# Kernel optimization log

Hardware: AMD Instinct MI355X
Metric: run time of the kernel (lower is better)

The kernel has to match this reference:

```python
import jax, jax.numpy as jnp
import numpy as np

N_K = 20000; N_E = 50000; N_U = 100000; EMB = 128
E_UND = 200000; E_EK = 400000; E_EU = 600000


def _gat(h, W, a, src, dst, n):
    """RCD GraphLayer: single-head GAT with edge softmax over incoming edges."""
    z = h @ W                                  # [N, d]
    d = z.shape[1]
    el = z @ a[:d]                             # src contribution to attn logit
    er = z @ a[d:]                             # dst contribution
    e = jax.nn.leaky_relu(el[src] + er[dst], 0.01)   # [E]
    m = jax.ops.segment_max(e, dst, num_segments=n)
    m = jnp.where(jnp.isfinite(m), m, 0.0)     # guard zero-degree nodes
    ex = jnp.exp(e - m[dst])
    s = jax.ops.segment_sum(ex, dst, num_segments=n)
    alpha = ex / s[dst]                        # per-dst softmax weights [E]
    return jax.ops.segment_sum(alpha[:, None] * z[src], dst, num_segments=n)


def setup_inputs() -> dict:
    key = jax.random.key(0)
    ks = jax.random.split(key, 32)
    sc = 1.0 / np.sqrt(EMB)
    inp = {
        'kn_emb': jax.random.normal(ks[0], (N_K, EMB), jnp.float32),
        'exer_emb': jax.random.normal(ks[1], (N_E, EMB), jnp.float32),
        'all_stu_emb': jax.random.normal(ks[2], (N_U, EMB), jnp.float32),
        'und_src': jax.random.randint(ks[3], (E_UND,), 0, N_K),
        'und_dst': jax.random.randint(ks[4], (E_UND,), 0, N_K),
        'ek_src': jax.random.randint(ks[5], (E_EK,), 0, N_E),
        'ek_dst': jax.random.randint(ks[6], (E_EK,), 0, N_K),
        'eu_src': jax.random.randint(ks[7], (E_EU,), 0, N_E),
        'eu_dst': jax.random.randint(ks[8], (E_EU,), 0, N_U),
        'W_und': jax.random.normal(ks[9], (EMB, EMB), jnp.float32) * sc,
        'a_und': jax.random.normal(ks[10], (2 * EMB,), jnp.float32) * sc,
        'W_ek': jax.random.normal(ks[11], (EMB, EMB), jnp.float32) * sc,
        'a_ek': jax.random.normal(ks[12], (2 * EMB,), jnp.float32) * sc,
        'W_ke': jax.random.normal(ks[13], (EMB, EMB), jnp.float32) * sc,
        'a_ke': jax.random.normal(ks[14], (2 * EMB,), jnp.float32) * sc,
        'W_eu': jax.random.normal(ks[15], (EMB, EMB), jnp.float32) * sc,
        'a_eu': jax.random.normal(ks[16], (2 * EMB,), jnp.float32) * sc,
        'W_ue': jax.random.normal(ks[17], (EMB, EMB), jnp.float32) * sc,
        'a_ue': jax.random.normal(ks[18], (2 * EMB,), jnp.float32) * sc,
        'k_fc2_w': jax.random.normal(ks[19], (2 * EMB,), jnp.float32) * sc,
        'k_fc2_b': jnp.zeros((1,), jnp.float32),
        'k_fc3_w': jax.random.normal(ks[20], (2 * EMB,), jnp.float32) * sc,
        'k_fc3_b': jnp.zeros((1,), jnp.float32),
        'e_fc1_w': jax.random.normal(ks[21], (2 * EMB,), jnp.float32) * sc,
        'e_fc1_b': jnp.zeros((1,), jnp.float32),
        'e_fc2_w': jax.random.normal(ks[22], (2 * EMB,), jnp.float32) * sc,
        'e_fc2_b': jnp.zeros((1,), jnp.float32),
    }
    return inp


def reference(kn_emb, exer_emb, all_stu_emb, und_src, und_dst, ek_src, ek_dst,
              eu_src, eu_dst, W_und, a_und, W_ek, a_ek, W_ke, a_ke, W_eu, a_eu,
              W_ue, a_ue, k_fc2_w, k_fc2_b, k_fc3_w, k_fc3_b, e_fc1_w, e_fc1_b,
              e_fc2_w, e_fc2_b):
    d = EMB
    # 1) undirected GAT on knowledge graph
    k_und = _gat(kn_emb, W_und, a_und, und_src, und_dst, N_K)
    # 2) exercise<->knowledge graphs on concatenated [exer; kn] nodes
    ek_nodes = jnp.concatenate([exer_emb, kn_emb], axis=0)
    e2k = _gat(ek_nodes, W_ek, a_ek, ek_src, ek_dst + N_E, N_E + N_K)
    k2e = _gat(ek_nodes, W_ke, a_ke, ek_dst + N_E, ek_src, N_E + N_K)
    # 3) exercise<->student graphs on concatenated [exer; stu] nodes
    eu_nodes = jnp.concatenate([exer_emb, all_stu_emb], axis=0)
    e2u = _gat(eu_nodes, W_eu, a_eu, eu_src, eu_dst + N_E, N_E + N_U)
    u2e = _gat(eu_nodes, W_ue, a_ue, eu_dst + N_E, eu_src, N_E + N_U)
    # knowledge fusion: attention-weighted residual combination
    A = kn_emb; C = k_und; D = e2k[N_E:]
    s2 = A @ k_fc2_w[:d] + C @ k_fc2_w[d:] + k_fc2_b[0]
    s3 = A @ k_fc3_w[:d] + D @ k_fc3_w[d:] + k_fc3_b[0]
    sk = jax.nn.softmax(jnp.stack([s2, s3], axis=1), axis=1)
    kn_out = A + sk[:, 0:1] * C + sk[:, 1:2] * D
    # exercise fusion
    Ae = exer_emb; B = k2e[:N_E]; Ce = u2e[:N_E]
    s1 = Ae @ e_fc1_w[:d] + B @ e_fc1_w[d:] + e_fc1_b[0]
    s2e = Ae @ e_fc2_w[:d] + Ce @ e_fc2_w[d:] + e_fc2_b[0]
    se = jax.nn.softmax(jnp.stack([s1, s2e], axis=1), axis=1)
    exer_out = Ae + se[:, 0:1] * B + se[:, 1:2] * Ce
    # student residual
    stu_out = all_stu_emb + e2u[N_E:]
    return (kn_out, exer_out, stu_out)
```

## Files before the change

kernel.cpp:

```cpp
#include <hip/hip_runtime.h>

#define N_K 20000
#define N_E 50000
#define N_U 100000
#define E_TOT 2200000
#define N_TOT 240000
#define KB1 0
#define KB2 20000
#define KB3 40000
#define KB4 90000
#define KB5 190000
#define NBKT 726
#define EPB 8192
#define NBLKA 269
#define APAD 272
#define KN_B 1250
#define EX_B 3125
#define ST_B 6250

typedef unsigned short u16;
typedef unsigned int u32;
typedef __bf16 bf16x8 __attribute__((ext_vector_type(8)));
typedef float f32x4 __attribute__((ext_vector_type(4)));

__device__ __forceinline__ float bf2f(u16 v){
    union { u32 u; float f; } x; x.u = ((u32)v) << 16; return x.f;
}
__device__ __forceinline__ u16 f2bf(float f){
    union { float f; u32 u; } x; x.f = f;
    u32 r = x.u + 0x7FFFu + ((x.u >> 16) & 1u);
    return (u16)(r >> 16);
}
__device__ __forceinline__ float leaky_exp(float x){
    x = x >= 0.f ? x : 0.01f*x;
    return __expf(x);
}

__device__ __forceinline__ int bucket_of(int key){
    if (key < 20000)  return key >> 8;
    if (key < 40000)  return 79  + ((key - 20000) >> 7);
    if (key < 90000)  return 236 + ((key - 40000) >> 9);
    if (key < 190000) return 334 + ((key - 90000) >> 9);
    return 530 + ((key - 190000) >> 8);
}
__device__ __forceinline__ void bucket_info(int b, int& kb, int& w, int& r){
    if (b < 79){       r=0; kb = b << 8;                 w = min(256, 20000  - kb); }
    else if (b < 236){ r=1; kb = 20000 + ((b-79)  << 7); w = min(128, 40000  - kb); }
    else if (b < 334){ r=2; kb = 40000 + ((b-236) << 9); w = min(512, 90000  - kb); }
    else if (b < 530){ r=3; kb = 90000 + ((b-334) << 9); w = min(512, 190000 - kb); }
    else {             r=4; kb = 190000 + ((b-530) << 8); w = min(256, 240000 - kb); }
}
__device__ __forceinline__ int edge_key(int e,
    const int* ud, const int* es, const int* ed, const int* vs, const int* vd){
    if (e < 200000)  return ud[e];
    if (e < 600000)  return 20000  + ed[e-200000];
    if (e < 1000000) return 40000  + es[e-600000];
    if (e < 1600000) return 90000  + vd[e-1000000];
    return 190000 + vs[e-1600000];
}
__device__ __forceinline__ int edge_src(int e,
    const int* us, const int* es, const int* ed, const int* vs, const int* vd){
    if (e < 200000)  return us[e];
    if (e < 600000)  return es[e-200000];
    if (e < 1000000) return ed[e-600000];
    if (e < 1600000) return vs[e-1000000];
    return vd[e-1600000];
}

__global__ __launch_bounds__(256) void prep_w(
    const float* W0, const float* W1, const float* W2, const float* W3, const float* W4,
    const float* a0, const float* a1, const float* a2, const float* a3, const float* a4,
    float* __restrict__ vecs, u16* __restrict__ Wf)
{
    int bid = blockIdx.x;
    if (bid < 320){
        int o = bid*4 + (threadIdx.x >> 6);
        int lane = threadIdx.x & 63;
        int which = o / 640, rem = o - which*640, g = rem >> 7, k = rem & 127;
        const float* W = g==0?W0:g==1?W1:g==2?W2:g==3?W3:W4;
        const float* a = g==0?a0:g==1?a1:g==2?a2:g==3?a3:a4;
        const float* av = a + which*128;
        int c = lane*2;
        float s = W[k*128 + c]*av[c] + W[k*128 + c + 1]*av[c+1];
        #pragma unroll
        for (int m = 32; m; m >>= 1) s += __shfl_xor(s, m);
        if (lane == 0) vecs[(which*5 + g)*128 + k] = s;
    } else {
        int t = (bid - 320)*256 + threadIdx.x;
        int g = t / 2048, i = t - g*2048;
        const float* W = g==0?W0:g==1?W1:g==2?W2:g==3?W3:W4;
        int lane = i & 63, tt = i >> 6, ks = tt & 3, ct = tt >> 2;
        int kbase = ks*32 + (lane>>4)*8;
        int c = ct*16 + (lane&15);
        #pragma unroll
        for (int j = 0; j < 8; ++j)
            Wf[g*16384 + i*8 + j] = f2bf(W[(kbase+j)*128 + c]);
    }
}

template<int WBF>
__global__ __launch_bounds__(256) void conv_all(
    const float* __restrict__ kn, const float* __restrict__ exer, const float* __restrict__ stu,
    u16* __restrict__ knb, u16* __restrict__ exerb, u16* __restrict__ stub,
    const float* __restrict__ vecs,
    float* __restrict__ el1, float* __restrict__ el2, float* __restrict__ el3,
    float* __restrict__ el4, float* __restrict__ el5, float* __restrict__ erc)
{
    int w = (int)((blockIdx.x*(u32)blockDim.x + threadIdx.x) >> 6);
    int lane = threadIdx.x & 63;
    if (w >= 170000) return;
    const float* h; u16* hb; int local, nd;
    const float *v0,*v1,*v2,*v3;
    float *o0,*o1,*o2,*o3;
    if (w < 20000){
        local = w; h = kn; hb = knb; nd = 4;
        v0=vecs+0;    v1=vecs+640;  v2=vecs+768;  v3=vecs+256;
        o0=el1; o1=erc+KB1; o2=erc+KB2; o3=el3;
    } else if (w < 70000){
        local = w - 20000; h = exer; hb = exerb; nd = 4;
        v0=vecs+128;  v1=vecs+896;  v2=vecs+384;  v3=vecs+1152;
        o0=el2; o1=erc+KB3; o2=el4; o3=erc+KB5;
    } else {
        local = w - 70000; h = stu; hb = stub; nd = 2;
        v0=vecs+1024; v1=vecs+512;  v2=vecs;      v3=vecs;
        o0=erc+KB4; o1=el5; o2=nullptr; o3=nullptr;
    }
    float2 hv = *(const float2*)(h + (size_t)local*128 + lane*2);
    if (WBF)
        *(u32*)(hb + (size_t)local*128 + lane*2) = (u32)f2bf(hv.x) | ((u32)f2bf(hv.y) << 16);
    int c = lane*2;
    float d0 = hv.x*v0[c] + hv.y*v0[c+1];
    float d1 = hv.x*v1[c] + hv.y*v1[c+1];
    float d2 = hv.x*v2[c] + hv.y*v2[c+1];
    float d3 = hv.x*v3[c] + hv.y*v3[c+1];
    #pragma unroll
    for (int o = 32; o; o >>= 1){
        d0 += __shfl_xor(d0, o); d1 += __shfl_xor(d1, o);
        d2 += __shfl_xor(d2, o); d3 += __shfl_xor(d3, o);
    }
    if (lane == 0){
        o0[local] = d0; o1[local] = d1;
        if (nd == 4){ o2[local] = d2; o3[local] = d3; }
    }
}

__global__ __launch_bounds__(256) void bkt_hist(
    const int* __restrict__ ud, const int* __restrict__ es, const int* __restrict__ ed,
    const int* __restrict__ vs, const int* __restrict__ vd, int* __restrict__ hist)
{
    __shared__ int h[NBKT];
    for (int i = threadIdx.x; i < NBKT; i += 256) h[i] = 0;
    __syncthreads();
    int base = blockIdx.x * EPB;
    #pragma unroll 4
    for (int it = 0; it < EPB/256; ++it){
        int e = base + it*256 + threadIdx.x;
        if (e < E_TOT){
            int key = edge_key(e, ud, es, ed, vs, vd);
            atomicAdd(&h[bucket_of(key)], 1);
        }
    }
    __syncthreads();
    for (int i = threadIdx.x; i < NBKT; i += 256)
        hist[i*APAD + blockIdx.x] = h[i];
}

__global__ __launch_bounds__(512) void bkt_scan1(int* __restrict__ hist, int* __restrict__ btot)
{
    __shared__ int sm[512];
    int t = threadIdx.x;
    int v = (t < NBLKA) ? hist[blockIdx.x*APAD + t] : 0;
    sm[t] = v; __syncthreads();
    #pragma unroll
    for (int d = 1; d < 512; d <<= 1){
        int x = (t >= d) ? sm[t-d] : 0;
        __syncthreads();
        sm[t] += x;
        __syncthreads();
    }
    if (t < NBLKA) hist[blockIdx.x*APAD + t] = sm[t] - v;
    if (t == 511) btot[blockIdx.x] = sm[511];
}

__global__ __launch_bounds__(1024) void bkt_scan2(const int* __restrict__ btot, int* __restrict__ bbase)
{
    __shared__ int sm[1024];
    int t = threadIdx.x;
    int v = (t < NBKT) ? btot[t] : 0;
    sm[t] = v; __syncthreads();
    #pragma unroll
    for (int d = 1; d < 1024; d <<= 1){
        int x = (t >= d) ? sm[t-d] : 0;
        __syncthreads();
        sm[t] += x;
        __syncthreads();
    }
    if (t < NBKT) bbase[t] = sm[t] - v;
}

__global__ __launch_bounds__(256) void bkt_scatter(
    const int* __restrict__ us, const int* __restrict__ ud,
    const int* __restrict__ es, const int* __restrict__ ed,
    const int* __restrict__ vs, const int* __restrict__ vd,
    const int* __restrict__ hist, const int* __restrict__ bbase,
    uint2* __restrict__ rec)
{
    __shared__ int cur[NBKT];
    for (int i = threadIdx.x; i < NBKT; i += 256)
        cur[i] = bbase[i] + hist[i*APAD + blockIdx.x];
    __syncthreads();
    int base = blockIdx.x * EPB;
    #pragma unroll 4
    for (int it = 0; it < EPB/256; ++it){
        int e = base + it*256 + threadIdx.x;
        if (e < E_TOT){
            int key = edge_key(e, ud, es, ed, vs, vd);
            int src = edge_src(e, us, es, ed, vs, vd);
            int pos = atomicAdd(&cur[bucket_of(key)], 1);
            rec[pos] = make_uint2((u32)src, (u32)key);
        }
    }
}

__global__ __launch_bounds__(512) void bkt_finalize(const uint2* __restrict__ rec,
    const int* __restrict__ bbase, const int* __restrict__ btot,
    const float* __restrict__ erc,
    const float* __restrict__ el1, const float* __restrict__ el2,
    const float* __restrict__ el3, const float* __restrict__ el4,
    const float* __restrict__ el5,
    int* __restrict__ cnt, int* __restrict__ offA, int2* __restrict__ sorted2)
{
    __shared__ int   h[512];
    __shared__ float s[512];
    __shared__ float ercs[512];
    __shared__ int   sm[512];
    __shared__ int   curk[512];
    int b = blockIdx.x, t = threadIdx.x;
    int kb, w, r;
    bucket_info(b, kb, w, r);
    h[t] = 0; s[t] = 0.f;
    if (t < w) ercs[t] = erc[kb + t];
    __syncthreads();
    const float* el = r==0?el1 : r==1?el2 : r==2?el3 : r==3?el4 : el5;
    int start = bbase[b], n = btot[b];
    for (int i = t; i < n; i += 512){
        uint2 rc = rec[start + i];
        int local = (int)rc.y - kb;
        atomicAdd(&h[local], 1);
        atomicAdd(&s[local], leaky_exp(el[rc.x] + ercs[local]));
    }
    __syncthreads();
    int hv = h[t];
    if (t < w) cnt[kb + t] = hv;
    sm[t] = hv; __syncthreads();
    #pragma unroll
    for (int d = 1; d < 512; d <<= 1){
        int x = (t >= d) ? sm[t-d] : 0;
        __syncthreads();
        sm[t] += x;
        __syncthreads();
    }
    int pos0 = start + sm[t] - hv;
    if (t < w) offA[kb + t] = pos0;
    curk[t] = pos0;
    __syncthreads();
    for (int i = t; i < n; i += 512){
        uint2 rc = rec[start + i];
        int local = (int)rc.y - kb;
        float alpha = leaky_exp(el[rc.x] + ercs[local]) / s[local];
        int pos = atomicAdd(&curk[local], 1);
        sorted2[pos] = make_int2((int)rc.x, __float_as_int(alpha));
    }
}

template<int BF>
__global__ __launch_bounds__(256) void agg_gemm_epi(
    const int* __restrict__ cnt, const int* __restrict__ offA, const int2* __restrict__ sorted2,
    const void* __restrict__ hk, const void* __restrict__ he, const void* __restrict__ hs,
    const u16* __restrict__ Wf,
    const float* __restrict__ kfc2w, const float* __restrict__ kfc2b,
    const float* __restrict__ kfc3w, const float* __restrict__ kfc3b,
    const float* __restrict__ efc1w, const float* __restrict__ efc1b,
    const float* __restrict__ efc2w, const float* __restrict__ efc2b,
    float* __restrict__ out)
{
    __shared__ u16 ldsC[16*136];
    __shared__ u16 ldsD[16*136];
    __shared__ float sred2[16], sred3[16], p2s[16], p3s[16];

    int bid = blockIdx.x;
    int wave = threadIdx.x >> 6, lane = threadIdx.x & 63;
    int kind, node0, keyC, keyD;
    const void *hC, *hD, *Aseg;
    const u16 *wc, *wd;
    const float *w2, *b2, *w3, *b3;
    float* outp;
    if (bid < KN_B){
        kind=0; node0 = bid*16;
        keyC = KB1 + node0; keyD = KB2 + node0;
        hC = hk; hD = he; Aseg = hk;
        wc = Wf; wd = Wf + 16384;
        w2=kfc2w; b2=kfc2b; w3=kfc3w; b3=kfc3b;
        outp = out;
    } else if (bid < KN_B + EX_B){
        kind=0; node0 = (bid - KN_B)*16;
        keyC = KB3 + node0; keyD = KB5 + node0;
        hC = hk; hD = hs; Aseg = he;
        wc = Wf + 2*16384; wd = Wf + 4*16384;
        w2=efc1w; b2=efc1b; w3=efc2w; b3=efc2b;
        outp = out + (size_t)N_K*128;
    } else {
        kind=1; node0 = (bid - KN_B - EX_B)*16;
        keyC = KB4 + node0; keyD = 0;
        hC = he; hD = nullptr; Aseg = hs;
        wc = Wf + 3*16384; wd = nullptr;
        w2=nullptr; b2=nullptr; w3=nullptr; b3=nullptr;
        outp = out + (size_t)(N_K + N_E)*128;
    }

    int rpw = (kind == 0) ? 8 : 4;
    for (int rr = 0; rr < rpw; ++rr){
        int c = wave*rpw + rr;
        int seg = c >> 4, nd = c & 15;
        int key = (seg == 0 ? keyC : keyD) + nd;
        const u32* hb32 = (const u32*)(seg == 0 ? hC : hD);
        const float2* hf2 = (const float2*)(seg == 0 ? hC : hD);
        int deg = cnt[key], start = offA[key];
        float a0 = 0.f, a1 = 0.f;
        int i = 0;
        for (; i + 8 <= deg; i += 8){
            int2 w[8];
            #pragma unroll
            for (int j = 0; j < 8; ++j) w[j] = sorted2[start+i+j];
            if (BF){
                u32 hv[8];
                #pragma unroll
                for (int j = 0; j < 8; ++j) hv[j] = hb32[(size_t)w[j].x*64 + lane];
                #pragma unroll
                for (int j = 0; j < 8; ++j){
                    float al = __int_as_float(w[j].y);
                    a0 = fmaf(al, bf2f((u16)hv[j]), a0);
                    a1 = fmaf(al, bf2f((u16)(hv[j]>>16)), a1);
                }
            } else {
                float2 hv[8];
                #pragma unroll
                for (int j = 0; j < 8; ++j) hv[j] = hf2[(size_t)w[j].x*64 + lane];
                #pragma unroll
                for (int j = 0; j < 8; ++j){
                    float al = __int_as_float(w[j].y);
                    a0 = fmaf(al, hv[j].x, a0);
                    a1 = fmaf(al, hv[j].y, a1);
                }
            }
        }
        for (; i + 4 <= deg; i += 4){
            int2 w[4];
            #pragma unroll
            for (int j = 0; j < 4; ++j) w[j] = sorted2[start+i+j];
            if (BF){
                u32 hv[4];
                #pragma unroll
                for (int j = 0; j < 4; ++j) hv[j] = hb32[(size_t)w[j].x*64 + lane];
                #pragma unroll
                for (int j = 0; j < 4; ++j){
                    float al = __int_as_float(w[j].y);
                    a0 = fmaf(al, bf2f((u16)hv[j]), a0);
                    a1 = fmaf(al, bf2f((u16)(hv[j]>>16)), a1);
                }
            } else {
                float2 hv[4];
                #pragma unroll
                for (int j = 0; j < 4; ++j) hv[j] = hf2[(size_t)w[j].x*64 + lane];
                #pragma unroll
                for (int j = 0; j < 4; ++j){
                    float al = __int_as_float(w[j].y);
                    a0 = fmaf(al, hv[j].x, a0);
                    a1 = fmaf(al, hv[j].y, a1);
                }
            }
        }
        for (; i < deg; ++i){
            int2 w = sorted2[start + i];
            float al = __int_as_float(w.y);
            if (BF){
                u32 hv = hb32[(size_t)w.x*64 + lane];
                a0 = fmaf(al, bf2f((u16)hv), a0);
                a1 = fmaf(al, bf2f((u16)(hv>>16)), a1);
            } else {
                float2 hv = hf2[(size_t)w.x*64 + lane];
                a0 = fmaf(al, hv.x, a0);
                a1 = fmaf(al, hv.y, a1);
            }
        }
        u16* dstl = (seg == 0 ? ldsC : ldsD) + nd*136 + lane*2;
        *(u32*)dstl = (u32)f2bf(a0) | ((u32)f2bf(a1) << 16);
    }
    if (threadIdx.x < 16){ sred2[threadIdx.x] = 0.f; sred3[threadIdx.x] = 0.f; }
    __syncthreads();

    int colb = lane & 15, rlo = (lane >> 4)*4;
    const float* Af = (const float*)Aseg;
    const u16*   Ab = (const u16*)Aseg;

    bf16x8 afC[4];
    #pragma unroll
    for (int ks = 0; ks < 4; ++ks)
        afC[ks] = *(const bf16x8*)(ldsC + (lane & 15)*136 + ks*32 + (lane >> 4)*8);
    f32x4 accC[2];
    accC[0] = (f32x4){0.f,0.f,0.f,0.f}; accC[1] = (f32x4){0.f,0.f,0.f,0.f};
    #pragma unroll
    for (int ci = 0; ci < 2; ++ci){
        int ct = wave*2 + ci;
        #pragma unroll
        for (int ks = 0; ks < 4; ++ks){
            bf16x8 bfr = *(const bf16x8*)(wc + ((ct*4+ks)*64 + lane)*8);
            accC[ci] = __builtin_amdgcn_mfma_f32_16x16x32_bf16(afC[ks], bfr, accC[ci], 0, 0, 0);
        }
    }

    if (kind == 1){
        #pragma unroll
        for (int ci = 0; ci < 2; ++ci){
            int ct = wave*2 + ci;
            #pragma unroll
            for (int j = 0; j < 4; ++j){
                size_t idx = (size_t)(node0 + rlo + j)*128 + ct*16 + colb;
                float av = BF ? bf2f(Ab[idx]) : Af[idx];
                outp[idx] = accC[ci][j] + av;
            }
        }
        return;
    }

    bf16x8 afD[4];
    #pragma unroll
    for (int ks = 0; ks < 4; ++ks)
        afD[ks] = *(const bf16x8*)(ldsD + (lane & 15)*136 + ks*32 + (lane >> 4)*8);
    f32x4 accD[2];
    accD[0] = (f32x4){0.f,0.f,0.f,0.f}; accD[1] = (f32x4){0.f,0.f,0.f,0.f};
    #pragma unroll
    for (int ci = 0; ci < 2; ++ci){
        int ct = wave*2 + ci;
        #pragma unroll
        for (int ks = 0; ks < 4; ++ks){
            bf16x8 bfr = *(const bf16x8*)(wd + ((ct*4+ks)*64 + lane)*8);
            accD[ci] = __builtin_amdgcn_mfma_f32_16x16x32_bf16(afD[ks], bfr, accD[ci], 0, 0, 0);
        }
    }

    float aA[2][4];
    float s2p[4] = {0.f,0.f,0.f,0.f}, s3p[4] = {0.f,0.f,0.f,0.f};
    #pragma unroll
    for (int ci = 0; ci < 2; ++ci){
        int ct = wave*2 + ci;
        float w2l = w2[ct*16 + colb], w2h = w2[128 + ct*16 + colb];
        float w3l = w3[ct*16 + colb], w3h = w3[128 + ct*16 + colb];
        #pragma unroll
        for (int j = 0; j < 4; ++j){
            size_t idx = (size_t)(node0 + rlo + j)*128 + ct*16 + colb;
            float av = BF ? bf2f(Ab[idx]) : Af[idx];
            aA[ci][j] = av;
            s2p[j] = fmaf(av, w2l, fmaf(accC[ci][j], w2h, s2p[j]));
            s3p[j] = fmaf(av, w3l, fmaf(accD[ci][j], w3h, s3p[j]));
        }
    }
    #pragma unroll
    for (int m = 8; m; m >>= 1)
        #pragma unroll
        for (int j = 0; j < 4; ++j){
            s2p[j] += __shfl_xor(s2p[j], m);
            s3p[j] += __shfl_xor(s3p[j], m);
        }
    if (colb == 0){
        #pragma unroll
        for (int j = 0; j < 4; ++j){
            atomicAdd(&sred2[rlo + j], s2p[j]);
            atomicAdd(&sred3[rlo + j], s3p[j]);
        }
    }
    __syncthreads();
    if (threadIdx.x < 16){
        float s2 = sred2[threadIdx.x] + b2[0];
        float s3 = sred3[threadIdx.x] + b3[0];
        float mx = fmaxf(s2, s3);
        float e2 = __expf(s2 - mx), e3 = __expf(s3 - mx);
        float inv = 1.f/(e2 + e3);
        p2s[threadIdx.x] = e2*inv;
        p3s[threadIdx.x] = e3*inv;
    }
    __syncthreads();
    #pragma unroll
    for (int ci = 0; ci < 2; ++ci){
        int ct = wave*2 + ci;
        #pragma unroll
        for (int j = 0; j < 4; ++j){
            int row = rlo + j;
            size_t idx = (size_t)(node0 + row)*128 + ct*16 + colb;
            outp[idx] = aA[ci][j] + p2s[row]*accC[ci][j] + p3s[row]*accD[ci][j];
        }
    }
}

extern "C" void kernel_launch(void* const* d_in, const int* in_sizes, int n_in,
                              void* d_out, int out_size, void* d_ws, size_t ws_size,
                              hipStream_t stream)
{
    (void)in_sizes; (void)n_in; (void)out_size;
    const float* kn   = (const float*)d_in[0];
    const float* exer = (const float*)d_in[1];
    const float* stu  = (const float*)d_in[2];
    const int* und_src = (const int*)d_in[3];
    const int* und_dst = (const int*)d_in[4];
    const int* ek_src  = (const int*)d_in[5];
    const int* ek_dst  = (const int*)d_in[6];
    const int* eu_src  = (const int*)d_in[7];
    const int* eu_dst  = (const int*)d_in[8];
    const float* W_und = (const float*)d_in[9];  const float* a_und = (const float*)d_in[10];
    const float* W_ek  = (const float*)d_in[11]; const float* a_ek  = (const float*)d_in[12];
    const float* W_ke  = (const float*)d_in[13]; const float* a_ke  = (const float*)d_in[14];
    const float* W_eu  = (const float*)d_in[15]; const float* a_eu  = (const float*)d_in[16];
    const float* W_ue  = (const float*)d_in[17]; const float* a_ue  = (const float*)d_in[18];
    const float* kfc2w = (const float*)d_in[19]; const float* kfc2b = (const float*)d_in[20];
    const float* kfc3w = (const float*)d_in[21]; const float* kfc3b = (const float*)d_in[22];
    const float* efc1w = (const float*)d_in[23]; const float* efc1b = (const float*)d_in[24];
    const float* efc2w = (const float*)d_in[25]; const float* efc2b = (const float*)d_in[26];

    char* base = (char*)d_ws;
    size_t off_b = 0;
    auto alloc = [&](size_t bytes)->char*{
        char* p = base + off_b;
        off_b += (bytes + 255) & ~(size_t)255;
        return p;
    };
    float* vecs = (float*)alloc(1280*4);
    u16*   Wf   = (u16*)  alloc(5*16384*2);
    float* el1 = (float*)alloc(N_K*4);
    float* el2 = (float*)alloc(N_E*4);
    float* el3 = (float*)alloc(N_K*4);
    float* el4 = (float*)alloc(N_E*4);
    float* el5 = (float*)alloc(N_U*4);
    float* erc = (float*)alloc((size_t)N_TOT*4);
    int* cnt  = (int*)alloc((size_t)N_TOT*4);
    int* offA = (int*)alloc((size_t)N_TOT*4);
    int* btot = (int*)alloc(NBKT*4);
    int* bbase= (int*)alloc(NBKT*4);
    int* hist = (int*)alloc((size_t)NBKT*APAD*4);
    uint2* rec = (uint2*)alloc((size_t)E_TOT*8);
    int2* sorted2 = (int2*)alloc((size_t)E_TOT*8);
    u16* knb   = (u16*)alloc((size_t)N_K*128*2);
    u16* exerb = (u16*)alloc((size_t)N_E*128*2);
    u16* stub  = (u16*)alloc((size_t)N_U*128*2);
    size_t need_bf = off_b;
    bool useBF = (ws_size >= need_bf);
    float* out = (float*)d_out;

    prep_w<<<360,256,0,stream>>>(W_und,W_ek,W_ke,W_eu,W_ue, a_und,a_ek,a_ke,a_eu,a_ue, vecs, Wf);

    if (useBF)
        conv_all<1><<<(170000+3)/4,256,0,stream>>>(kn, exer, stu, knb, exerb, stub, vecs,
                                                   el1, el2, el3, el4, el5, erc);
    else
        conv_all<0><<<(170000+3)/4,256,0,stream>>>(kn, exer, stu, knb, exerb, stub, vecs,
                                                   el1, el2, el3, el4, el5, erc);

    bkt_hist<<<NBLKA,256,0,stream>>>(und_dst, ek_src, ek_dst, eu_src, eu_dst, hist);
    bkt_scan1<<<NBKT,512,0,stream>>>(hist, btot);
    bkt_scan2<<<1,1024,0,stream>>>(btot, bbase);
    bkt_scatter<<<NBLKA,256,0,stream>>>(und_src, und_dst, ek_src, ek_dst, eu_src, eu_dst,
                                        hist, bbase, rec);
    bkt_finalize<<<NBKT,512,0,stream>>>(rec, bbase, btot, erc,
                                        el1, el2, el3, el4, el5,
                                        cnt, offA, sorted2);

    if (useBF){
        agg_gemm_epi<1><<<KN_B+EX_B+ST_B,256,0,stream>>>(cnt, offA, sorted2,
            knb, exerb, stub, Wf,
            kfc2w,kfc2b,kfc3w,kfc3b, efc1w,efc1b,efc2w,efc2b, out);
    } else {
        agg_gemm_epi<0><<<KN_B+EX_B+ST_B,256,0,stream>>>(cnt, offA, sorted2,
            kn, exer, stu, Wf,
            kfc2w,kfc2b,kfc3w,kfc3b, efc1w,efc1b,efc2w,efc2b, out);
    }
}
```

Measured before the change: 308.6 us.

## Gather neighbor features in FP8 and cache edge exponentials in finalize

Adds an FP8 (e4m3) copy of the node embeddings and uses it for the edge-weighted neighbor gather in the aggregation kernel, which halves the bytes fetched per gathered row compared with bf16. The bf16 copies are still used for the GEMM A operand. Separately, bkt_finalize now stores each edge's exp value in a new buffer instead of recomputing it, trading extra global traffic for less recomputation. FP8 lowers feature precision before the GEMM and may hurt accuracy. The fp8 and bf16 stores in conv_all also both remain, so that pass writes more data.

After: 299.4 us. 1.03x faster.

```diff
diff --git a/kernel.cpp b/kernel.cpp
--- a/kernel.cpp
+++ b/kernel.cpp
@@ -1,4 +1,5 @@
 #include <hip/hip_runtime.h>
+#include <hip/hip_fp8.h>
 
 #define N_K 20000
 #define N_E 50000
@@ -20,6 +21,7 @@
 
 typedef unsigned short u16;
 typedef unsigned int u32;
+typedef unsigned char u8;
 typedef __bf16 bf16x8 __attribute__((ext_vector_type(8)));
 typedef float f32x4 __attribute__((ext_vector_type(4)));
 
@@ -34,6 +36,28 @@
 __device__ __forceinline__ float leaky_exp(float x){
     x = x >= 0.f ? x : 0.01f*x;
     return __expf(x);
+}
+__device__ __forceinline__ u16 fp8pk(float a, float b){
+#if __has_builtin(__builtin_amdgcn_cvt_pk_fp8_f32)
+    return (u16)__builtin_amdgcn_cvt_pk_fp8_f32(a, b, 0, false);
+#else
+    __hip_fp8_e4m3 qa(a), qb(b);
+    return (u16)qa.__x | ((u16)qb.__x << 8);
+#endif
+}
+__device__ __forceinline__ float fp8lo(u32 w){
+#if __has_builtin(__builtin_amdgcn_cvt_f32_fp8)
+    return __builtin_amdgcn_cvt_f32_fp8((int)w, 0);
+#else
+    __hip_fp8_e4m3 q; q.__x = (u8)(w & 0xFF); return (float)q;
+#endif
+}
+__device__ __forceinline__ float fp8hi(u32 w){
+#if __has_builtin(__builtin_amdgcn_cvt_f32_fp8)
+    return __builtin_amdgcn_cvt_f32_fp8((int)w, 1);
+#else
+    __hip_fp8_e4m3 q; q.__x = (u8)((w >> 8) & 0xFF); return (float)q;
+#endif
 }
 
 __device__ __forceinline__ int bucket_of(int key){
@@ -102,6 +126,7 @@
 __global__ __launch_bounds__(256) void conv_all(
     const float* __restrict__ kn, const float* __restrict__ exer, const float* __restrict__ stu,
     u16* __restrict__ knb, u16* __restrict__ exerb, u16* __restrict__ stub,
+    u8* __restrict__ knf, u8* __restrict__ exerf, u8* __restrict__ stuf,
     const float* __restrict__ vecs,
     float* __restrict__ el1, float* __restrict__ el2, float* __restrict__ el3,
     float* __restrict__ el4, float* __restrict__ el5, float* __restrict__ erc)
@@ -109,25 +134,27 @@
     int w = (int)((blockIdx.x*(u32)blockDim.x + threadIdx.x) >> 6);
     int lane = threadIdx.x & 63;
     if (w >= 170000) return;
-    const float* h; u16* hb; int local, nd;
+    const float* h; u16* hb; u8* hf; int local, nd;
     const float *v0,*v1,*v2,*v3;
     float *o0,*o1,*o2,*o3;
     if (w < 20000){
-        local = w; h = kn; hb = knb; nd = 4;
+        local = w; h = kn; hb = knb; hf = knf; nd = 4;
         v0=vecs+0;    v1=vecs+640;  v2=vecs+768;  v3=vecs+256;
         o0=el1; o1=erc+KB1; o2=erc+KB2; o3=el3;
     } else if (w < 70000){
-        local = w - 20000; h = exer; hb = exerb; nd = 4;
+        local = w - 20000; h = exer; hb = exerb; hf = exerf; nd = 4;
         v0=vecs+128;  v1=vecs+896;  v2=vecs+384;  v3=vecs+1152;
         o0=el2; o1=erc+KB3; o2=el4; o3=erc+KB5;
     } else {
-        local = w - 70000; h = stu; hb = stub; nd = 2;
+        local = w - 70000; h = stu; hb = stub; hf = stuf; nd = 2;
         v0=vecs+1024; v1=vecs+512;  v2=vecs;      v3=vecs;
         o0=erc+KB4; o1=el5; o2=nullptr; o3=nullptr;
     }
     float2 hv = *(const float2*)(h + (size_t)local*128 + lane*2);
-    if (WBF)
+    if (WBF){
         *(u32*)(hb + (size_t)local*128 + lane*2) = (u32)f2bf(hv.x) | ((u32)f2bf(hv.y) << 16);
+        *(u16*)(hf + (size_t)local*128 + lane*2) = fp8pk(hv.x, hv.y);
+    }
     int c = lane*2;
     float d0 = hv.x*v0[c] + hv.y*v0[c+1];
     float d1 = hv.x*v1[c] + hv.y*v1[c+1];
@@ -227,7 +254,7 @@
     const float* __restrict__ erc,
     const float* __restrict__ el1, const float* __restrict__ el2,
     const float* __restrict__ el3, const float* __restrict__ el4,
-    const float* __restrict__ el5,
+    const float* __restrict__ el5, float* __restrict__ evb,
     int* __restrict__ cnt, int* __restrict__ offA, int2* __restrict__ sorted2)
 {
     __shared__ int   h[512];
@@ -246,8 +273,10 @@
     for (int i = t; i < n; i += 512){
         uint2 rc = rec[start + i];
         int local = (int)rc.y - kb;
+        float ev = leaky_exp(el[rc.x] + ercs[local]);
+        evb[start + i] = ev;
         atomicAdd(&h[local], 1);
-        atomicAdd(&s[local], leaky_exp(el[rc.x] + ercs[local]));
+        atomicAdd(&s[local], ev);
     }
     __syncthreads();
     int hv = h[t];
@@ -267,7 +296,7 @@
     for (int i = t; i < n; i += 512){
         uint2 rc = rec[start + i];
         int local = (int)rc.y - kb;
-        float alpha = leaky_exp(el[rc.x] + ercs[local]) / s[local];
+        float alpha = evb[start + i] / s[local];
         int pos = atomicAdd(&curk[local], 1);
         sorted2[pos] = make_int2((int)rc.x, __float_as_int(alpha));
     }
@@ -276,7 +305,8 @@
 template<int BF>
 __global__ __launch_bounds__(256) void agg_gemm_epi(
     const int* __restrict__ cnt, const int* __restrict__ offA, const int2* __restrict__ sorted2,
-    const void* __restrict__ hk, const void* __restrict__ he, const void* __restrict__ hs,
+    const void* __restrict__ hk8, const void* __restrict__ he8, const void* __restrict__ hs8,
+    const void* __restrict__ knA, const void* __restrict__ exerA, const void* __restrict__ stuA,
     const u16* __restrict__ Wf,
     const float* __restrict__ kfc2w, const float* __restrict__ kfc2b,
     const float* __restrict__ kfc3w, const float* __restrict__ kfc3b,
@@ -298,21 +328,21 @@
     if (bid < KN_B){
         kind=0; node0 = bid*16;
         keyC = KB1 + node0; keyD = KB2 + node0;
-        hC = hk; hD = he; Aseg = hk;
+        hC = hk8; hD = he8; Aseg = knA;
         wc = Wf; wd = Wf + 16384;
         w2=kfc2w; b2=kfc2b; w3=kfc3w; b3=kfc3b;
         outp = out;
     } else if (bid < KN_B + EX_B){
         kind=0; node0 = (bid - KN_B)*16;
         keyC = KB3 + node0; keyD = KB5 + node0;
-        hC = hk; hD = hs; Aseg = he;
+        hC = hk8; hD = hs8; Aseg = exerA;
         wc = Wf + 2*16384; wd = Wf + 4*16384;
         w2=efc1w; b2=efc1b; w3=efc2w; b3=efc2b;
         outp = out + (size_t)N_K*128;
     } else {
         kind=1; node0 = (bid - KN_B - EX_B)*16;
         keyC = KB4 + node0; keyD = 0;
-        hC = he; hD = nullptr; Aseg = hs;
+        hC = he8; hD = nullptr; Aseg = stuA;
         wc = Wf + 3*16384; wd = nullptr;
         w2=nullptr; b2=nullptr; w3=nullptr; b3=nullptr;
         outp = out + (size_t)(N_K + N_E)*128;
@@ -323,7 +353,7 @@
         int c = wave*rpw + rr;
         int seg = c >> 4, nd = c & 15;
         int key = (seg == 0 ? keyC : keyD) + nd;
-        const u32* hb32 = (const u32*)(seg == 0 ? hC : hD);
+        const u16* h16 = (const u16*)(seg == 0 ? hC : hD);
         const float2* hf2 = (const float2*)(seg == 0 ? hC : hD);
         int deg = cnt[key], start = offA[key];
         float a0 = 0.f, a1 = 0.f;
@@ -335,12 +365,12 @@
             if (BF){
                 u32 hv[8];
                 #pragma unroll
-                for (int j = 0; j < 8; ++j) hv[j] = hb32[(size_t)w[j].x*64 + lane];
+                for (int j = 0; j < 8; ++j) hv[j] = h16[(size_t)w[j].x*64 + lane];
                 #pragma unroll
                 for (int j = 0; j < 8; ++j){
                     float al = __int_as_float(w[j].y);
-                    a0 = fmaf(al, bf2f((u16)hv[j]), a0);
-                    a1 = fmaf(al, bf2f((u16)(hv[j]>>16)), a1);
+                    a0 = fmaf(al, fp8lo(hv[j]), a0);
+                    a1 = fmaf(al, fp8hi(hv[j]), a1);
                 }
             } else {
                 float2 hv[8];
@@ -361,12 +391,12 @@
             if (BF){
                 u32 hv[4];
                 #pragma unroll
-                for (int j = 0; j < 4; ++j) hv[j] = hb32[(size_t)w[j].x*64 + lane];
+                for (int j = 0; j < 4; ++j) hv[j] = h16[(size_t)w[j].x*64 + lane];
                 #pragma unroll
                 for (int j = 0; j < 4; ++j){
                     float al = __int_as_float(w[j].y);
-                    a0 = fmaf(al, bf2f((u16)hv[j]), a0);
-                    a1 = fmaf(al, bf2f((u16)(hv[j]>>16)), a1);
+                    a0 = fmaf(al, fp8lo(hv[j]), a0);
+                    a1 = fmaf(al, fp8hi(hv[j]), a1);
                 }
             } else {
                 float2 hv[4];
@@ -384,9 +414,9 @@
             int2 w = sorted2[start + i];
             float al = __int_as_float(w.y);
             if (BF){
-                u32 hv = hb32[(size_t)w.x*64 + lane];
-                a0 = fmaf(al, bf2f((u16)hv), a0);
-                a1 = fmaf(al, bf2f((u16)(hv>>16)), a1);
+                u32 hv = h16[(size_t)w.x*64 + lane];
+                a0 = fmaf(al, fp8lo(hv), a0);
+                a1 = fmaf(al, fp8hi(hv), a1);
             } else {
                 float2 hv = hf2[(size_t)w.x*64 + lane];
                 a0 = fmaf(al, hv.x, a0);
@@ -547,10 +577,14 @@
     int* bbase= (int*)alloc(NBKT*4);
     int* hist = (int*)alloc((size_t)NBKT*APAD*4);
     uint2* rec = (uint2*)alloc((size_t)E_TOT*8);
+    float* evb = (float*)alloc((size_t)E_TOT*4);
     int2* sorted2 = (int2*)alloc((size_t)E_TOT*8);
     u16* knb   = (u16*)alloc((size_t)N_K*128*2);
     u16* exerb = (u16*)alloc((size_t)N_E*128*2);
     u16* stub  = (u16*)alloc((size_t)N_U*128*2);
+    u8* knf   = (u8*)alloc((size_t)N_K*128);
+    u8* exerf = (u8*)alloc((size_t)N_E*128);
+    u8* stuf  = (u8*)alloc((size_t)N_U*128);
     size_t need_bf = off_b;
     bool useBF = (ws_size >= need_bf);
     float* out = (float*)d_out;
@@ -558,10 +592,12 @@
     prep_w<<<360,256,0,stream>>>(W_und,W_ek,W_ke,W_eu,W_ue, a_und,a_ek,a_ke,a_eu,a_ue, vecs, Wf);
 
     if (useBF)
-        conv_all<1><<<(170000+3)/4,256,0,stream>>>(kn, exer, stu, knb, exerb, stub, vecs,
+        conv_all<1><<<(170000+3)/4,256,0,stream>>>(kn, exer, stu, knb, exerb, stub,
+                                                   knf, exerf, stuf, vecs,
                                                    el1, el2, el3, el4, el5, erc);
     else
-        conv_all<0><<<(170000+3)/4,256,0,stream>>>(kn, exer, stu, knb, exerb, stub, vecs,
+        conv_all<0><<<(170000+3)/4,256,0,stream>>>(kn, exer, stu, knb, exerb, stub,
+                                                   knf, exerf, stuf, vecs,
                                                    el1, el2, el3, el4, el5, erc);
 
     bkt_hist<<<NBLKA,256,0,stream>>>(und_dst, ek_src, ek_dst, eu_src, eu_dst, hist);
@@ -570,16 +606,16 @@
     bkt_scatter<<<NBLKA,256,0,stream>>>(und_src, und_dst, ek_src, ek_dst, eu_src, eu_dst,
                                         hist, bbase, rec);
     bkt_finalize<<<NBKT,512,0,stream>>>(rec, bbase, btot, erc,
-                                        el1, el2, el3, el4, el5,
+                                        el1, el2, el3, el4, el5, evb,
                                         cnt, offA, sorted2);
 
     if (useBF){
         agg_gemm_epi<1><<<KN_B+EX_B+ST_B,256,0,stream>>>(cnt, offA, sorted2,
-            knb, exerb, stub, Wf,
+            knf, exerf, stuf, knb, exerb, stub, Wf,
             kfc2w,kfc2b,kfc3w,kfc3b, efc1w,efc1b,efc2w,efc2b, out);
     } else {
         agg_gemm_epi<0><<<KN_B+EX_B+ST_B,256,0,stream>>>(cnt, offA, sorted2,
-            kn, exer, stu, Wf,
+            kn, exer, stu, kn, exer, stu, Wf,
             kfc2w,kfc2b,kfc3w,kfc3b, efc1w,efc1b,efc2w,efc2b, out);
     }
 }
```

## Interleave two destination nodes per wave in gather and cache edge exponentials

Applied to the files above, without the earlier changes.

The aggregation loop now processes two destination nodes at once per wave, issuing the neighbour-row gathers for both together. This raises memory-level parallelism on the latency-bound random gather, at the cost of more registers and extra tail loops. Separately, bkt_finalize stores each edge's exp value in a new buffer so the second pass reuses it instead of regathering el and recomputing the exponential. That trades an extra 4-byte write and read per edge for the skipped gather and math.

After: 286.0 us. 1.08x faster.

```diff
diff --git a/kernel.cpp b/kernel.cpp
--- a/kernel.cpp
+++ b/kernel.cpp
@@ -227,7 +227,7 @@
     const float* __restrict__ erc,
     const float* __restrict__ el1, const float* __restrict__ el2,
     const float* __restrict__ el3, const float* __restrict__ el4,
-    const float* __restrict__ el5,
+    const float* __restrict__ el5, float* __restrict__ evb,
     int* __restrict__ cnt, int* __restrict__ offA, int2* __restrict__ sorted2)
 {
     __shared__ int   h[512];
@@ -246,8 +246,10 @@
     for (int i = t; i < n; i += 512){
         uint2 rc = rec[start + i];
         int local = (int)rc.y - kb;
+        float ev = leaky_exp(el[rc.x] + ercs[local]);
+        evb[start + i] = ev;
         atomicAdd(&h[local], 1);
-        atomicAdd(&s[local], leaky_exp(el[rc.x] + ercs[local]));
+        atomicAdd(&s[local], ev);
     }
     __syncthreads();
     int hv = h[t];
@@ -267,7 +269,7 @@
     for (int i = t; i < n; i += 512){
         uint2 rc = rec[start + i];
         int local = (int)rc.y - kb;
-        float alpha = leaky_exp(el[rc.x] + ercs[local]) / s[local];
+        float alpha = evb[start + i] / s[local];
         int pos = atomicAdd(&curk[local], 1);
         sorted2[pos] = make_int2((int)rc.x, __float_as_int(alpha));
     }
@@ -319,45 +321,60 @@
     }
 
     int rpw = (kind == 0) ? 8 : 4;
-    for (int rr = 0; rr < rpw; ++rr){
-        int c = wave*rpw + rr;
-        int seg = c >> 4, nd = c & 15;
-        int key = (seg == 0 ? keyC : keyD) + nd;
+    for (int rr = 0; rr < rpw; rr += 2){
+        int cA = wave*rpw + rr;
+        int seg = cA >> 4, ndA = cA & 15;
+        int keyA = (seg == 0 ? keyC : keyD) + ndA;
         const u32* hb32 = (const u32*)(seg == 0 ? hC : hD);
         const float2* hf2 = (const float2*)(seg == 0 ? hC : hD);
-        int deg = cnt[key], start = offA[key];
-        float a0 = 0.f, a1 = 0.f;
-        int i = 0;
-        for (; i + 8 <= deg; i += 8){
-            int2 w[8];
+        int degA = cnt[keyA],     startA = offA[keyA];
+        int degB = cnt[keyA + 1], startB = offA[keyA + 1];
+        float a0A=0.f, a1A=0.f, a0B=0.f, a1B=0.f;
+        int iA = 0, iB = 0;
+        while (iA + 4 <= degA && iB + 4 <= degB){
+            int2 wA[4], wB[4];
             #pragma unroll
-            for (int j = 0; j < 8; ++j) w[j] = sorted2[start+i+j];
+            for (int j = 0; j < 4; ++j){
+                wA[j] = sorted2[startA + iA + j];
+                wB[j] = sorted2[startB + iB + j];
+            }
             if (BF){
-                u32 hv[8];
-                #pragma unroll
-                for (int j = 0; j < 8; ++j) hv[j] = hb32[(size_t)w[j].x*64 + lane];
-                #pragma unroll
-                for (int j = 0; j < 8; ++j){
-                    float al = __int_as_float(w[j].y);
-                    a0 = fmaf(al, bf2f((u16)hv[j]), a0);
-                    a1 = fmaf(al, bf2f((u16)(hv[j]>>16)), a1);
+                u32 hvA[4], hvB[4];
+                #pragma unroll
+                for (int j = 0; j < 4; ++j){
+                    hvA[j] = hb32[(size_t)wA[j].x*64 + lane];
+                    hvB[j] = hb32[(size_t)wB[j].x*64 + lane];
+                }
+                #pragma unroll
+                for (int j = 0; j < 4; ++j){
+                    float alA = __int_as_float(wA[j].y);
+                    float alB = __int_as_float(wB[j].y);
+                    a0A = fmaf(alA, bf2f((u16)hvA[j]), a0A);
+                    a1A = fmaf(alA, bf2f((u16)(hvA[j]>>16)), a1A);
+                    a0B = fmaf(alB, bf2f((u16)hvB[j]), a0B);
+                    a1B = fmaf(alB, bf2f((u16)(hvB[j]>>16)), a1B);
                 }
             } else {
-                float2 hv[8];
-                #pragma unroll
-                for (int j = 0; j < 8; ++j) hv[j] = hf2[(size_t)w[j].x*64 + lane];
-                #pragma unroll
-                for (int j = 0; j < 8; ++j){
-                    float al = __int_as_float(w[j].y);
-                    a0 = fmaf(al, hv[j].x, a0);
-                    a1 = fmaf(al, hv[j].y, a1);
+                float2 hvA[4], hvB[4];
+                #pragma unroll
+                for (int j = 0; j < 4; ++j){
+                    hvA[j] = hf2[(size_t)wA[j].x*64 + lane];
+                    hvB[j] = hf2[(size_t)wB[j].x*64 + lane];
+                }
+                #pragma unroll
+                for (int j = 0; j < 4; ++j){
+                    float alA = __int_as_float(wA[j].y);
+                    float alB = __int_as_float(wB[j].y);
+                    a0A = fmaf(alA, hvA[j].x, a0A); a1A = fmaf(alA, hvA[j].y, a1A);
+                    a0B = fmaf(alB, hvB[j].x, a0B); a1B = fmaf(alB, hvB[j].y, a1B);
                 }
             }
-        }
-        for (; i + 4 <= deg; i += 4){
+            iA += 4; iB += 4;
+        }
+        for (; iA + 4 <= degA; iA += 4){
             int2 w[4];
             #pragma unroll
-            for (int j = 0; j < 4; ++j) w[j] = sorted2[start+i+j];
+            for (int j = 0; j < 4; ++j) w[j] = sorted2[startA + iA + j];
             if (BF){
                 u32 hv[4];
                 #pragma unroll
@@ -365,8 +382,8 @@
                 #pragma unroll
                 for (int j = 0; j < 4; ++j){
                     float al = __int_as_float(w[j].y);
-                    a0 = fmaf(al, bf2f((u16)hv[j]), a0);
-                    a1 = fmaf(al, bf2f((u16)(hv[j]>>16)), a1);
+                    a0A = fmaf(al, bf2f((u16)hv[j]), a0A);
+                    a1A = fmaf(al, bf2f((u16)(hv[j]>>16)), a1A);
                 }
             } else {
                 float2 hv[4];
@@ -375,26 +392,75 @@
                 #pragma unroll
                 for (int j = 0; j < 4; ++j){
                     float al = __int_as_float(w[j].y);
-                    a0 = fmaf(al, hv[j].x, a0);
-                    a1 = fmaf(al, hv[j].y, a1);
+                    a0A = fmaf(al, hv[j].x, a0A); a1A = fmaf(al, hv[j].y, a1A);
                 }
             }
         }
-        for (; i < deg; ++i){
-            int2 w = sorted2[start + i];
-            float al = __int_as_float(w.y);
+        for (; iB + 4 <= degB; iB += 4){
+            int2 w[4];
+            #pragma unroll
+            for (int j = 0; j < 4; ++j) w[j] = sorted2[startB + iB + j];
             if (BF){
-                u32 hv = hb32[(size_t)w.x*64 + lane];
-                a0 = fmaf(al, bf2f((u16)hv), a0);
-                a1 = fmaf(al, bf2f((u16)(hv>>16)), a1);
+                u32 hv[4];
+                #pragma unroll
+                for (int j = 0; j < 4; ++j) hv[j] = hb32[(size_t)w[j].x*64 + lane];
+                #pragma unroll
+                for (int j = 0; j < 4; ++j){
+                    float al = __int_as_float(w[j].y);
+                    a0B = fmaf(al, bf2f((u16)hv[j]), a0B);
+                    a1B = fmaf(al, bf2f((u16)(hv[j]>>16)), a1B);
+                }
             } else {
-                float2 hv = hf2[(size_t)w.x*64 + lane];
-                a0 = fmaf(al, hv.x, a0);
-                a1 = fmaf(al, hv.y, a1);
+                float2 hv[4];
+                #pragma unroll
+                for (int j = 0; j < 4; ++j) hv[j] = hf2[(size_t)w[j].x*64 + lane];
+                #pragma unroll
+                for (int j = 0; j < 4; ++j){
+                    float al = __int_as_float(w[j].y);
+                    a0B = fmaf(al, hv[j].x, a0B); a1B = fmaf(al, hv[j].y, a1B);
+                }
             }
         }
-        u16* dstl = (seg == 0 ? ldsC : ldsD) + nd*136 + lane*2;
-        *(u32*)dstl = (u32)f2bf(a0) | ((u32)f2bf(a1) << 16);
+        while (iA < degA || iB < degB){
+            bool dA = iA < degA, dB = iB < degB;
+            int2 wA, wB;
+            if (dA) wA = sorted2[startA + iA];
+            if (dB) wB = sorted2[startB + iB];
+            if (BF){
+                u32 hvA = 0, hvB = 0;
+                if (dA) hvA = hb32[(size_t)wA.x*64 + lane];
+                if (dB) hvB = hb32[(size_t)wB.x*64 + lane];
+                if (dA){
+                    float al = __int_as_float(wA.y);
+                    a0A = fmaf(al, bf2f((u16)hvA), a0A);
+                    a1A = fmaf(al, bf2f((u16)(hvA>>16)), a1A);
+                    ++iA;
+                }
+                if (dB){
+                    float al = __int_as_float(wB.y);
+                    a0B = fmaf(al, bf2f((u16)hvB), a0B);
+                    a1B = fmaf(al, bf2f((u16)(hvB>>16)), a1B);
+                    ++iB;
+                }
+            } else {
+                float2 hvA = make_float2(0.f,0.f), hvB = make_float2(0.f,0.f);
+                if (dA) hvA = hf2[(size_t)wA.x*64 + lane];
+                if (dB) hvB = hf2[(size_t)wB.x*64 + lane];
+                if (dA){
+                    float al = __int_as_float(wA.y);
+                    a0A = fmaf(al, hvA.x, a0A); a1A = fmaf(al, hvA.y, a1A);
+                    ++iA;
+                }
+                if (dB){
+                    float al = __int_as_float(wB.y);
+                    a0B = fmaf(al, hvB.x, a0B); a1B = fmaf(al, hvB.y, a1B);
+                    ++iB;
+                }
+            }
+        }
+        u16* ldsSeg = (seg == 0 ? ldsC : ldsD);
+        *(u32*)(ldsSeg + ndA*136 + lane*2)     = (u32)f2bf(a0A) | ((u32)f2bf(a1A) << 16);
+        *(u32*)(ldsSeg + (ndA+1)*136 + lane*2) = (u32)f2bf(a0B) | ((u32)f2bf(a1B) << 16);
     }
     if (threadIdx.x < 16){ sred2[threadIdx.x] = 0.f; sred3[threadIdx.x] = 0.f; }
     __syncthreads();
@@ -547,6 +613,7 @@
     int* bbase= (int*)alloc(NBKT*4);
     int* hist = (int*)alloc((size_t)NBKT*APAD*4);
     uint2* rec = (uint2*)alloc((size_t)E_TOT*8);
+    float* evb = (float*)alloc((size_t)E_TOT*4);
     int2* sorted2 = (int2*)alloc((size_t)E_TOT*8);
     u16* knb   = (u16*)alloc((size_t)N_K*128*2);
     u16* exerb = (u16*)alloc((size_t)N_E*128*2);
@@ -570,7 +637,7 @@
     bkt_scatter<<<NBLKA,256,0,stream>>>(und_src, und_dst, ek_src, ek_dst, eu_src, eu_dst,
                                         hist, bbase, rec);
     bkt_finalize<<<NBKT,512,0,stream>>>(rec, bbase, btot, erc,
-                                        el1, el2, el3, el4, el5,
+                                        el1, el2, el3, el4, el5, evb,
                                         cnt, offA, sorted2);
 
     if (useBF){
```

## Precompute edge exp in scatter and gather 4 edges per wave with 16B loads

Applied to the files above, without the earlier changes.

The scatter pass now computes each edge's leaky-exp attention score and packs the local node index into the high bits of the src field, so finalize no longer gathers el/erc and recomputes the exponential twice. The aggregation loop is restructured so each wave handles two nodes at once, with four lane groups each taking a different edge and loading a full 128-element row slice in 16-byte chunks, followed by a cross-group shuffle reduction. This aims to cut per-edge load instructions and expose more memory parallelism in the gather. The risks are extra shuffle work and wasted lanes on low-degree tails, and the packing assumes src indices fit in 17 bits.

New measurement: 303.4 us. About the same (-1.7%).

```diff
diff --git a/kernel.cpp b/kernel.cpp
--- a/kernel.cpp
+++ b/kernel.cpp
@@ -42,6 +42,13 @@
     if (key < 90000)  return 236 + ((key - 40000) >> 9);
     if (key < 190000) return 334 + ((key - 90000) >> 9);
     return 530 + ((key - 190000) >> 8);
+}
+__device__ __forceinline__ int local_of(int key){
+    if (key < 20000)  return key & 255;
+    if (key < 40000)  return (key - 20000) & 127;
+    if (key < 90000)  return (key - 40000) & 511;
+    if (key < 190000) return (key - 90000) & 511;
+    return (key - 190000) & 255;
 }
 __device__ __forceinline__ void bucket_info(int b, int& kb, int& w, int& r){
     if (b < 79){       r=0; kb = b << 8;                 w = min(256, 20000  - kb); }
@@ -203,6 +210,9 @@
     const int* __restrict__ es, const int* __restrict__ ed,
     const int* __restrict__ vs, const int* __restrict__ vd,
     const int* __restrict__ hist, const int* __restrict__ bbase,
+    const float* __restrict__ el1, const float* __restrict__ el2,
+    const float* __restrict__ el3, const float* __restrict__ el4,
+    const float* __restrict__ el5, const float* __restrict__ erc,
     uint2* __restrict__ rec)
 {
     __shared__ int cur[NBKT];
@@ -216,38 +226,35 @@
         if (e < E_TOT){
             int key = edge_key(e, ud, es, ed, vs, vd);
             int src = edge_src(e, us, es, ed, vs, vd);
+            const float* el = (e < 200000) ? el1 : (e < 600000) ? el2 :
+                              (e < 1000000) ? el3 : (e < 1600000) ? el4 : el5;
+            float ev = leaky_exp(el[src] + erc[key]);
+            int local = local_of(key);
             int pos = atomicAdd(&cur[bucket_of(key)], 1);
-            rec[pos] = make_uint2((u32)src, (u32)key);
+            rec[pos] = make_uint2((u32)src | ((u32)local << 17), __float_as_uint(ev));
         }
     }
 }
 
 __global__ __launch_bounds__(512) void bkt_finalize(const uint2* __restrict__ rec,
     const int* __restrict__ bbase, const int* __restrict__ btot,
-    const float* __restrict__ erc,
-    const float* __restrict__ el1, const float* __restrict__ el2,
-    const float* __restrict__ el3, const float* __restrict__ el4,
-    const float* __restrict__ el5,
     int* __restrict__ cnt, int* __restrict__ offA, int2* __restrict__ sorted2)
 {
     __shared__ int   h[512];
     __shared__ float s[512];
-    __shared__ float ercs[512];
     __shared__ int   sm[512];
     __shared__ int   curk[512];
     int b = blockIdx.x, t = threadIdx.x;
     int kb, w, r;
     bucket_info(b, kb, w, r);
     h[t] = 0; s[t] = 0.f;
-    if (t < w) ercs[t] = erc[kb + t];
-    __syncthreads();
-    const float* el = r==0?el1 : r==1?el2 : r==2?el3 : r==3?el4 : el5;
+    __syncthreads();
     int start = bbase[b], n = btot[b];
     for (int i = t; i < n; i += 512){
         uint2 rc = rec[start + i];
-        int local = (int)rc.y - kb;
+        int local = (int)(rc.x >> 17);
         atomicAdd(&h[local], 1);
-        atomicAdd(&s[local], leaky_exp(el[rc.x] + ercs[local]));
+        atomicAdd(&s[local], __uint_as_float(rc.y));
     }
     __syncthreads();
     int hv = h[t];
@@ -266,10 +273,10 @@
     __syncthreads();
     for (int i = t; i < n; i += 512){
         uint2 rc = rec[start + i];
-        int local = (int)rc.y - kb;
-        float alpha = leaky_exp(el[rc.x] + ercs[local]) / s[local];
+        int local = (int)(rc.x >> 17);
+        float alpha = __uint_as_float(rc.y) / s[local];
         int pos = atomicAdd(&curk[local], 1);
-        sorted2[pos] = make_int2((int)rc.x, __float_as_int(alpha));
+        sorted2[pos] = make_int2((int)(rc.x & 0x1FFFFu), __float_as_int(alpha));
     }
 }
 
@@ -290,6 +297,7 @@
 
     int bid = blockIdx.x;
     int wave = threadIdx.x >> 6, lane = threadIdx.x & 63;
+    int g = lane >> 4, s = lane & 15;
     int kind, node0, keyC, keyD;
     const void *hC, *hD, *Aseg;
     const u16 *wc, *wd;
@@ -319,82 +327,72 @@
     }
 
     int rpw = (kind == 0) ? 8 : 4;
-    for (int rr = 0; rr < rpw; ++rr){
-        int c = wave*rpw + rr;
-        int seg = c >> 4, nd = c & 15;
-        int key = (seg == 0 ? keyC : keyD) + nd;
-        const u32* hb32 = (const u32*)(seg == 0 ? hC : hD);
-        const float2* hf2 = (const float2*)(seg == 0 ? hC : hD);
-        int deg = cnt[key], start = offA[key];
-        float a0 = 0.f, a1 = 0.f;
-        int i = 0;
-        for (; i + 8 <= deg; i += 8){
-            int2 w[8];
-            #pragma unroll
-            for (int j = 0; j < 8; ++j) w[j] = sorted2[start+i+j];
-            if (BF){
-                u32 hv[8];
-                #pragma unroll
-                for (int j = 0; j < 8; ++j) hv[j] = hb32[(size_t)w[j].x*64 + lane];
-                #pragma unroll
-                for (int j = 0; j < 8; ++j){
-                    float al = __int_as_float(w[j].y);
-                    a0 = fmaf(al, bf2f((u16)hv[j]), a0);
-                    a1 = fmaf(al, bf2f((u16)(hv[j]>>16)), a1);
-                }
-            } else {
-                float2 hv[8];
-                #pragma unroll
-                for (int j = 0; j < 8; ++j) hv[j] = hf2[(size_t)w[j].x*64 + lane];
-                #pragma unroll
-                for (int j = 0; j < 8; ++j){
-                    float al = __int_as_float(w[j].y);
-                    a0 = fmaf(al, hv[j].x, a0);
-                    a1 = fmaf(al, hv[j].y, a1);
-                }
-            }
-        }
-        for (; i + 4 <= deg; i += 4){
-            int2 w[4];
-            #pragma unroll
-            for (int j = 0; j < 4; ++j) w[j] = sorted2[start+i+j];
-            if (BF){
-                u32 hv[4];
-                #pragma unroll
-                for (int j = 0; j < 4; ++j) hv[j] = hb32[(size_t)w[j].x*64 + lane];
-                #pragma unroll
-                for (int j = 0; j < 4; ++j){
-                    float al = __int_as_float(w[j].y);
-                    a0 = fmaf(al, bf2f((u16)hv[j]), a0);
-                    a1 = fmaf(al, bf2f((u16)(hv[j]>>16)), a1);
-                }
-            } else {
-                float2 hv[4];
-                #pragma unroll
-                for (int j = 0; j < 4; ++j) hv[j] = hf2[(size_t)w[j].x*64 + lane];
-                #pragma unroll
-                for (int j = 0; j < 4; ++j){
-                    float al = __int_as_float(w[j].y);
-                    a0 = fmaf(al, hv[j].x, a0);
-                    a1 = fmaf(al, hv[j].y, a1);
-                }
-            }
-        }
-        for (; i < deg; ++i){
-            int2 w = sorted2[start + i];
+    for (int rr = 0; rr < rpw; rr += 2){
+        int cA = wave*rpw + rr;
+        int seg = cA >> 4, ndA = cA & 15;
+        int keyA = (seg == 0 ? keyC : keyD) + ndA;
+        const u16* hb = (const u16*)(seg == 0 ? hC : hD);
+        const float4* hf = (const float4*)(seg == 0 ? hC : hD);
+        int degA = cnt[keyA],     startA = offA[keyA];
+        int degB = cnt[keyA + 1], startB = offA[keyA + 1];
+        float aA8[8], aB8[8];
+        #pragma unroll
+        for (int k = 0; k < 8; ++k){ aA8[k] = 0.f; aB8[k] = 0.f; }
+
+        auto chunk = [&](const int2* sp, float* acc){
+            int2 w = sp[g];
             float al = __int_as_float(w.y);
             if (BF){
-                u32 hv = hb32[(size_t)w.x*64 + lane];
-                a0 = fmaf(al, bf2f((u16)hv), a0);
-                a1 = fmaf(al, bf2f((u16)(hv>>16)), a1);
+                uint4 hv = *(const uint4*)(hb + (size_t)w.x*128 + s*8);
+                acc[0] = fmaf(al, bf2f((u16)hv.x), acc[0]);
+                acc[1] = fmaf(al, bf2f((u16)(hv.x>>16)), acc[1]);
+                acc[2] = fmaf(al, bf2f((u16)hv.y), acc[2]);
+                acc[3] = fmaf(al, bf2f((u16)(hv.y>>16)), acc[3]);
+                acc[4] = fmaf(al, bf2f((u16)hv.z), acc[4]);
+                acc[5] = fmaf(al, bf2f((u16)(hv.z>>16)), acc[5]);
+                acc[6] = fmaf(al, bf2f((u16)hv.w), acc[6]);
+                acc[7] = fmaf(al, bf2f((u16)(hv.w>>16)), acc[7]);
             } else {
-                float2 hv = hf2[(size_t)w.x*64 + lane];
-                a0 = fmaf(al, hv.x, a0);
-                a1 = fmaf(al, hv.y, a1);
+                const float4* rp = hf + (size_t)w.x*32 + s*2;
+                float4 p0 = rp[0], p1 = rp[1];
+                acc[0] = fmaf(al, p0.x, acc[0]); acc[1] = fmaf(al, p0.y, acc[1]);
+                acc[2] = fmaf(al, p0.z, acc[2]); acc[3] = fmaf(al, p0.w, acc[3]);
+                acc[4] = fmaf(al, p1.x, acc[4]); acc[5] = fmaf(al, p1.y, acc[5]);
+                acc[6] = fmaf(al, p1.z, acc[6]); acc[7] = fmaf(al, p1.w, acc[7]);
             }
-        }
-        u16* dstl = (seg == 0 ? ldsC : ldsD) + nd*136 + lane*2;
-        *(u32*)dstl = (u32)f2bf(a0) | ((u32)f2bf(a1) << 16);
+        };
+
+        int iA = 0, iB = 0;
+        while (iA + 4 <= degA && iB + 4 <= degB){
+            chunk(sorted2 + startA + iA, aA8);
+            chunk(sorted2 + startB + iB, aB8);
+            iA += 4; iB += 4;
+        }
+        for (; iA + 4 <= degA; iA += 4) chunk(sorted2 + startA + iA, aA8);
+        for (; iB + 4 <= degB; iB += 4) chunk(sorted2 + startB + iB, aB8);
+        int remA = degA - iA;
+        if (g < remA) chunk(sorted2 + startA + iA, aA8);
+        int remB = degB - iB;
+        if (g < remB) chunk(sorted2 + startB + iB, aB8);
+
+        #pragma unroll
+        for (int k = 0; k < 8; ++k){
+            aA8[k] += __shfl_xor(aA8[k], 16); aA8[k] += __shfl_xor(aA8[k], 32);
+            aB8[k] += __shfl_xor(aB8[k], 16); aB8[k] += __shfl_xor(aB8[k], 32);
+        }
+        u16* ldsSeg = (seg == 0 ? ldsC : ldsD);
+        if (lane < 16){
+            u32 p0 = (u32)f2bf(aA8[0]) | ((u32)f2bf(aA8[1]) << 16);
+            u32 p1 = (u32)f2bf(aA8[2]) | ((u32)f2bf(aA8[3]) << 16);
+            u32 p2 = (u32)f2bf(aA8[4]) | ((u32)f2bf(aA8[5]) << 16);
+            u32 p3 = (u32)f2bf(aA8[6]) | ((u32)f2bf(aA8[7]) << 16);
+            *(uint4*)(ldsSeg + ndA*136 + lane*8) = make_uint4(p0,p1,p2,p3);
+            u32 q0 = (u32)f2bf(aB8[0]) | ((u32)f2bf(aB8[1]) << 16);
+            u32 q1 = (u32)f2bf(aB8[2]) | ((u32)f2bf(aB8[3]) << 16);
+            u32 q2 = (u32)f2bf(aB8[4]) | ((u32)f2bf(aB8[5]) << 16);
+            u32 q3 = (u32)f2bf(aB8[6]) | ((u32)f2bf(aB8[7]) << 16);
+            *(uint4*)(ldsSeg + (ndA+1)*136 + lane*8) = make_uint4(q0,q1,q2,q3);
+        }
     }
     if (threadIdx.x < 16){ sred2[threadIdx.x] = 0.f; sred3[threadIdx.x] = 0.f; }
     __syncthreads();
@@ -568,10 +566,9 @@
     bkt_scan1<<<NBKT,512,0,stream>>>(hist, btot);
     bkt_scan2<<<1,1024,0,stream>>>(btot, bbase);
     bkt_scatter<<<NBLKA,256,0,stream>>>(und_src, und_dst, ek_src, ek_dst, eu_src, eu_dst,
-                                        hist, bbase, rec);
-    bkt_finalize<<<NBKT,512,0,stream>>>(rec, bbase, btot, erc,
-                                        el1, el2, el3, el4, el5,
-                                        cnt, offA, sorted2);
+                                        hist, bbase,
+                                        el1, el2, el3, el4, el5, erc, rec);
+    bkt_finalize<<<NBKT,512,0,stream>>>(rec, bbase, btot, cnt, offA, sorted2);
 
     if (useBF){
         agg_gemm_epi<1><<<KN_B+EX_B+ST_B,256,0,stream>>>(cnt, offA, sorted2,
```
